# Kernel optimization log

Hardware: AMD Instinct MI355X
Metric: run time of the kernel (lower is better)

Reference implementation:

```python
import jax, jax.numpy as jnp
import numpy as np

H, T, D = 16, 2048, 1024
DH = D // H  # 64


def setup_inputs() -> dict:
    key = jax.random.key(0)
    ks = jax.random.split(key, 6)
    state = jax.random.normal(ks[0], (H, DH, DH), jnp.float32) * 0.02  # per-head recurrent state
    x = jax.random.normal(ks[1], (T, D), jnp.float32)
    done = jax.random.uniform(ks[2], (T,)) < (4.0 / T)  # sparse episode-reset flags (bool)
    w_qkv = jax.random.normal(ks[3], (D, 3 * D), jnp.float32) / np.sqrt(D)
    b_qkv = jnp.zeros((3 * D,), jnp.float32)
    w_out = jax.random.normal(ks[4], (D, D), jnp.float32) / np.sqrt(D)
    b_out = jnp.zeros((D,), jnp.float32)
    return {"state": state, "x": x, "done": done, "w_qkv": w_qkv,
            "b_qkv": b_qkv, "w_out": w_out, "b_out": b_out}


def _mha_forward(state, x, done, w_qkv, b_qkv, w_out, b_out):
    # qkv projection; einops 'T (QKV H Dh) -> QKV H T Dh'
    qkv = (x @ w_qkv + b_qkv).reshape(T, 3, H, DH).transpose(1, 2, 0, 3)
    q, k, v = qkv[0], qkv[1], qkv[2]  # each (H, T, Dh)

    cum = jnp.cumsum(done.astype(jnp.int32))  # inclusive cumsum, as in done.cumsum()
    before_first = cum == 0            # tokens before first reset (attend to carried state)
    after_last = cum == cum[-1]        # tokens after last reset (feed new state)
    done_any = cum[-1] > 0

    # make_attn_mask(done): causal AND no reset index i with s < i <= t.
    # The scanned mask equals: causal & (cum[t] == cum[s]) (same-segment).
    t_idx = jnp.arange(T)
    mask = (t_idx[:, None] >= t_idx[None, :]) & (cum[:, None] == cum[None, :])  # (T, T)

    attn = jnp.where(mask[None], jnp.einsum('htd,hsd->hts', q, k), 0.0)  # mask * (q @ k.T)
    q_bef = q * before_first[None, :, None]
    out = jnp.einsum('hts,hsd->htd', attn, v) + jnp.einsum('htd,hde->hte', q_bef, state)

    k_aft = k * after_last[None, :, None]
    v_aft = v * after_last[None, :, None]
    s_new = jnp.einsum('htd,hte->hde', k_aft, v_aft)  # k_aft.T @ v_aft per head
    new_state = jnp.where(done_any, s_new, state + s_new)

    # 'H T Dh -> T (H Dh)' then output projection
    x_out = out.transpose(1, 0, 2).reshape(T, D) @ w_out + b_out
    return new_state, x_out


def reference(state, x, done, w_qkv, b_qkv, w_out, b_out):
    return _mha_forward(state, x, done, w_qkv, b_qkv, w_out, b_out)
```

## Files before the change

kernel.cpp:

```cpp
#include <hip/hip_runtime.h>

#define TT 2048
#define DD 1024
#define HH 16
#define DH 64
#define QKV_N 3072
#define QKW 2048

typedef __attribute__((ext_vector_type(8))) short bf16x8;
typedef __attribute__((ext_vector_type(4))) short short4v;
typedef __attribute__((ext_vector_type(4))) float f32x4;

__device__ inline short f2bf(float f) {
    union { float f; unsigned u; } v; v.f = f;
    unsigned r = v.u + 0x7fff + ((v.u >> 16) & 1);
    return (short)(r >> 16);
}

__device__ inline f32x4 mfma16(bf16x8 a, bf16x8 b, f32x4 c) {
    return __builtin_amdgcn_mfma_f32_16x16x32_bf16(a, b, c, 0, 0, 0);
}

__device__ __forceinline__ void gload16(const void* g, void* l) {
    __builtin_amdgcn_global_load_lds(
        (const __attribute__((address_space(1))) unsigned int*)g,
        (__attribute__((address_space(3))) unsigned int*)l, 16, 0, 0);
}

__device__ void transpose_tile(const float* __restrict__ in, short* __restrict__ out,
                               int R, int C, int r0, int c0, float (*tile)[65]) {
    int tid = threadIdx.x;
#pragma unroll
    for (int p = 0; p < 4; ++p) {
        int ch = tid + p * 256;
        int r = ch >> 4, c4 = (ch & 15) * 4;
        float4 v = *(const float4*)&in[(size_t)(r0 + r) * C + c0 + c4];
        tile[r][c4] = v.x; tile[r][c4 + 1] = v.y; tile[r][c4 + 2] = v.z; tile[r][c4 + 3] = v.w;
    }
    __syncthreads();
#pragma unroll
    for (int p = 0; p < 2; ++p) {
        int ch = tid + p * 256;
        int c = ch >> 3, r8 = (ch & 7) * 8;
        short tmp[8];
#pragma unroll
        for (int i = 0; i < 8; ++i) tmp[i] = f2bf(tile[r8 + i][c]);
        *(float4*)&out[(size_t)(c0 + c) * R + r0 + r8] = *(float4*)tmp;
    }
}

__global__ __launch_bounds__(256) void prep_kernel(const float* __restrict__ x,
                                                   const float* __restrict__ w_qkv,
                                                   const float* __restrict__ w_out,
                                                   const float* __restrict__ state,
                                                   const int* __restrict__ done,
                                                   short* __restrict__ x_bf,
                                                   short* __restrict__ wqT,
                                                   short* __restrict__ woT,
                                                   short* __restrict__ stT,
                                                   float* __restrict__ stout,
                                                   int* __restrict__ seg,
                                                   int* __restrict__ totalp,
                                                   int* __restrict__ aux) {
    __shared__ float tile[64][65];
    __shared__ int scanbuf[2048 + 512 + 1];
    int b = blockIdx.x;
    int tid = threadIdx.x;
    if (b < 1024) {
        int i = (b * 256 + tid) * 8;
        float4 a = *(const float4*)&x[i];
        float4 c = *(const float4*)&x[i + 4];
        short tmp[8] = {f2bf(a.x), f2bf(a.y), f2bf(a.z), f2bf(a.w),
                        f2bf(c.x), f2bf(c.y), f2bf(c.z), f2bf(c.w)};
        *(float4*)&x_bf[i] = *(float4*)tmp;
    } else if (b < 1792) {
        int bb = b - 1024;
        transpose_tile(w_qkv, wqT, DD, QKV_N, (bb & 15) * 64, (bb >> 4) * 64, tile);
    } else if (b < 2048) {
        int bb = b - 1792;
        transpose_tile(w_out, woT, DD, DD, (bb & 15) * 64, (bb >> 4) * 64, tile);
    } else if (b < 2064) {
        int h = b - 2048;
        transpose_tile(state + (size_t)h * 4096, stT + (size_t)h * 4096, DH, DH, 0, 0, tile);
    } else if (b < 2128) {
        __shared__ int anyf;
        if (tid == 0) anyf = 0;
        __syncthreads();
        int acc = 0;
#pragma unroll
        for (int i = 0; i < 8; ++i) acc |= done[tid * 8 + i];
        if (acc) anyf = 1;
        __syncthreads();
        int f = ((b - 2064) * 256 + tid) * 4;
        float4 v = anyf ? make_float4(0.f, 0.f, 0.f, 0.f) : *(const float4*)&state[f];
        *(float4*)&stout[f] = v;
    } else {
        int* segl = scanbuf;
        int* part = scanbuf + 2048;
        int* excl = scanbuf + 2304;
        int base = tid * 8;
        int local[8];
        int run = 0;
#pragma unroll
        for (int i = 0; i < 8; ++i) { run += (done[base + i] != 0) ? 1 : 0; local[i] = run; }
        part[tid] = run;
        __syncthreads();
        if (tid < 64) {
            int p4[4];
#pragma unroll
            for (int i = 0; i < 4; ++i) p4[i] = part[tid * 4 + i];
            int s = p4[0] + p4[1] + p4[2] + p4[3];
            int v = s;
#pragma unroll
            for (int off = 1; off < 64; off <<= 1) {
                int u = __shfl_up(v, off);
                if (tid >= off) v += u;
            }
            int ex = v - s;
#pragma unroll
            for (int i = 0; i < 4; ++i) { excl[tid * 4 + i] = ex; ex += p4[i]; }
            if (tid == 63) { totalp[0] = v; scanbuf[2560] = v; }
        }
        __syncthreads();
        int off = excl[tid];
#pragma unroll
        for (int i = 0; i < 8; ++i) {
            int sv = off + local[i];
            seg[base + i] = sv;
            segl[base + i] = sv;
        }
        __syncthreads();
        if (tid < 33) {
            int target = (tid < 32) ? segl[tid * 64] : scanbuf[2560];
            int lo = 0, hi = 2047;
            while (lo < hi) { int mid = (lo + hi) >> 1; if (segl[mid] >= target) hi = mid; else lo = mid + 1; }
            aux[tid] = lo >> 6;
        }
    }
}

__global__ __launch_bounds__(256) void gemm_qkv(const short* __restrict__ A,
                                                const short* __restrict__ BT,
                                                const float* __restrict__ bias,
                                                short* __restrict__ qk,
                                                short* __restrict__ vt) {
    __shared__ __align__(16) short As[2][2][128 * 32];
    __shared__ __align__(16) short Bs[2][2][128 * 32];
    const int K = DD;
    int tid = threadIdx.x;
    int wave = tid >> 6, lane = tid & 63;
    int quad = lane >> 4, l15 = lane & 15;
    int m0 = blockIdx.x * 128, n0 = blockIdx.y * 128;
    int wr = (wave >> 1) * 64, wc = (wave & 1) * 64;

    int srow = wave * 32 + (lane >> 2);
    int scol = (lane & 3) * 8;
    const short* Ag = A + (size_t)(m0 + srow) * K + scol;
    const short* Bg = BT + (size_t)(n0 + srow) * K + scol;

#pragma unroll
    for (int g = 0; g < 2; ++g)
#pragma unroll
        for (int ks = 0; ks < 2; ++ks) {
            gload16(Ag + (size_t)g * 16 * K + ks * 32, &As[0][ks][(wave * 32 + g * 16) * 32]);
            gload16(Bg + (size_t)g * 16 * K + ks * 32, &Bs[0][ks][(wave * 32 + g * 16) * 32]);
        }
    __syncthreads();

    f32x4 acc[4][4] = {};
    int cur = 0;
    for (int k0 = 0; k0 < K; k0 += 64, cur ^= 1) {
        if (k0 + 64 < K) {
#pragma unroll
            for (int g = 0; g < 2; ++g)
#pragma unroll
                for (int ks = 0; ks < 2; ++ks) {
                    gload16(Ag + (size_t)g * 16 * K + k0 + 64 + ks * 32,
                            &As[cur ^ 1][ks][(wave * 32 + g * 16) * 32]);
                    gload16(Bg + (size_t)g * 16 * K + k0 + 64 + ks * 32,
                            &Bs[cur ^ 1][ks][(wave * 32 + g * 16) * 32]);
                }
        }
#pragma unroll
        for (int ks = 0; ks < 2; ++ks) {
            bf16x8 af[4], bfr[4];
#pragma unroll
            for (int i = 0; i < 4; ++i) {
                af[i]  = *(const bf16x8*)&As[cur][ks][(wr + i * 16 + l15) * 32 + quad * 8];
                bfr[i] = *(const bf16x8*)&Bs[cur][ks][(wc + i * 16 + l15) * 32 + quad * 8];
            }
#pragma unroll
            for (int i = 0; i < 4; ++i)
#pragma unroll
                for (int j = 0; j < 4; ++j)
                    acc[i][j] = mfma16(af[i], bfr[j], acc[i][j]);
        }
        __syncthreads();
    }

    if (n0 < 2048) {
#pragma unroll
        for (int i = 0; i < 4; ++i)
#pragma unroll
            for (int j = 0; j < 4; ++j)
#pragma unroll
                for (int r = 0; r < 4; ++r) {
                    int row = m0 + wr + i * 16 + quad * 4 + r;
                    int col = n0 + wc + j * 16 + l15;
                    qk[(size_t)row * QKW + col] = f2bf(acc[i][j][r] + bias[col]);
                }
    } else {
#pragma unroll
        for (int j = 0; j < 4; ++j) {
            int col = n0 + wc + j * 16 + l15;
            float bv = bias[col];
            int eg = col - 2048;
            int hh = eg >> 6, e = eg & 63;
#pragma unroll
            for (int i = 0; i < 4; ++i) {
                int tb = m0 + wr + i * 16 + quad * 4;
                short4v pk;
#pragma unroll
                for (int r = 0; r < 4; ++r) pk[r] = f2bf(acc[i][j][r] + bv);
                *(short4v*)&vt[(size_t)hh * (DH * TT) + (size_t)e * TT + tb] = pk;
            }
        }
    }
}

__global__ __launch_bounds__(256) void attn_mfma(const short* __restrict__ qk,
                                                 const short* __restrict__ vt,
                                                 const short* __restrict__ stT,
                                                 const int* __restrict__ seg,
                                                 const int* __restrict__ totalp,
                                                 const int* __restrict__ aux,
                                                 short* __restrict__ outb,
                                                 float* __restrict__ nsout) {
    __shared__ __align__(16) short Qh[2][64 * 32];
    __shared__ __align__(16) short Kh[2][2][64 * 32];
    __shared__ __align__(16) short Vh[2][2][64 * 32];
    __shared__ __align__(16) short Ss[64 * 72];

    int h = blockIdx.x, tt = blockIdx.y, z = blockIdx.z;
    int t0 = tt * 64;
    int tid = threadIdx.x, wave = tid >> 6, lane = tid & 63;
    int quad = lane >> 4, l15 = lane & 15;
    int myt = wave * 16;
    const short* vbase = vt + (size_t)h * (DH * TT);

    if (z == 1) {
        if (tt < aux[32]) return;
        int total = totalp[0];
        int myd = wave * 16;
        short* K0 = Kh[0][0];
        short* K1 = Kh[0][1];
        bool keep = (seg[t0 + lane] == total);
        const short* src = qk + (size_t)(t0 + lane) * QKW + 1024 + h * DH + myd;
        union { float4 f; short s[8]; } u0, u1;
        u0.f = keep ? *(const float4*)src : make_float4(0.f, 0.f, 0.f, 0.f);
        u1.f = keep ? *(const float4*)(src + 8) : make_float4(0.f, 0.f, 0.f, 0.f);
        short* dst = (lane < 32) ? &K0[lane] : &K1[lane - 32];
#pragma unroll
        for (int i = 0; i < 8; ++i) {
            dst[(myd + i) * 32] = u0.s[i];
            dst[(myd + 8 + i) * 32] = u1.s[i];
        }
        bf16x8 a0 = *(const bf16x8*)&K0[(myd + l15) * 32 + quad * 8];
        bf16x8 a1 = *(const bf16x8*)&K1[(myd + l15) * 32 + quad * 8];
        f32x4 acc2[4] = {};
#pragma unroll
        for (int j = 0; j < 4; ++j) {
            const short* vrow = vbase + (size_t)(j * 16 + l15) * TT + t0 + quad * 8;
            bf16x8 b0 = *(const bf16x8*)vrow;
            bf16x8 b1 = *(const bf16x8*)(vrow + 32);
            acc2[j] = mfma16(a0, b0, acc2[j]);
            acc2[j] = mfma16(a1, b1, acc2[j]);
        }
        float* oh = nsout + (size_t)h * 4096;
#pragma unroll
        for (int j = 0; j < 4; ++j)
#pragma unroll
            for (int r = 0; r < 4; ++r)
                atomicAdd(&oh[(myd + quad * 4 + r) * DH + j * 16 + l15], acc2[j][r]);
        return;
    }

    int st0 = aux[tt];
    int sr = lane >> 2;
    int ch = lane & 3;
    const short* kg = qk + 1024 + h * DH;

    {
#pragma unroll
        for (int h2 = 0; h2 < 2; ++h2)
            gload16(qk + (size_t)(t0 + myt + sr) * QKW + h * DH + h2 * 32 + ch * 8,
                    &Qh[h2][myt * 32]);
        int s0 = st0 * 64;
        gload16(kg + (size_t)(s0 + myt + sr) * QKW + ch * 8,      &Kh[0][0][myt * 32]);
        gload16(kg + (size_t)(s0 + myt + sr) * QKW + 32 + ch * 8, &Kh[0][1][myt * 32]);
        gload16(vbase + (size_t)(myt + sr) * TT + s0 + ch * 8,    &Vh[0][0][myt * 32]);
        gload16(vbase + (size_t)(myt + sr) * TT + s0 + 32 + ch * 8, &Vh[0][1][myt * 32]);
    }
    __syncthreads();

    bf16x8 af[2];
#pragma unroll
    for (int h2 = 0; h2 < 2; ++h2)
        af[h2] = *(const bf16x8*)&Qh[h2][(myt + l15) * 32 + quad * 8];

    int t_val = t0 + myt + l15;
    int seg_lane = seg[t_val];

    f32x4 acc2[4] = {};
    if (seg[t0] == 0) {
        const short* sb = stT + (size_t)h * 4096;
#pragma unroll
        for (int j = 0; j < 4; ++j)
#pragma unroll
            for (int h2 = 0; h2 < 2; ++h2) {
                bf16x8 a = *(const bf16x8*)(sb + (j * 16 + l15) * 64 + h2 * 32 + quad * 8);
                acc2[j] = mfma16(a, af[h2], acc2[j]);
            }
        if (seg_lane != 0) {
#pragma unroll
            for (int j = 0; j < 4; ++j)
#pragma unroll
                for (int r = 0; r < 4; ++r) acc2[j][r] = 0.f;
        }
    }

    int p = 0;
    for (int st = st0; st <= tt; ++st, p ^= 1) {
        if (st != st0) __syncthreads();
        if (st + 1 <= tt) {
            int s1 = (st + 1) * 64;
            gload16(kg + (size_t)(s1 + myt + sr) * QKW + ch * 8,        &Kh[p ^ 1][0][myt * 32]);
            gload16(kg + (size_t)(s1 + myt + sr) * QKW + 32 + ch * 8,   &Kh[p ^ 1][1][myt * 32]);
            gload16(vbase + (size_t)(myt + sr) * TT + s1 + ch * 8,      &Vh[p ^ 1][0][myt * 32]);
            gload16(vbase + (size_t)(myt + sr) * TT + s1 + 32 + ch * 8, &Vh[p ^ 1][1][myt * 32]);
        }
        int s0 = st * 64;

        f32x4 sacc[4] = {};
#pragma unroll
        for (int j = 0; j < 4; ++j)
#pragma unroll
            for (int h2 = 0; h2 < 2; ++h2) {
                bf16x8 kb = *(const bf16x8*)&Kh[p][h2][(j * 16 + l15) * 32 + quad * 8];
                sacc[j] = mfma16(kb, af[h2], sacc[j]);
            }
        int4 seg4[4];
#pragma unroll
        for (int j = 0; j < 4; ++j)
            seg4[j] = *(const int4*)&seg[s0 + j * 16 + quad * 4];
#pragma unroll
        for (int j = 0; j < 4; ++j) {
            short4v pk;
#pragma unroll
            for (int r = 0; r < 4; ++r) {
                int s_val = s0 + j * 16 + quad * 4 + r;
                int sv = (r == 0) ? seg4[j].x : (r == 1) ? seg4[j].y : (r == 2) ? seg4[j].z : seg4[j].w;
                bool ok = (sv == seg_lane) && (s_val <= t_val);
                pk[r] = ok ? f2bf(sacc[j][r]) : (short)0;
            }
            *(short4v*)&Ss[(myt + l15) * 72 + j * 16 + quad * 4] = pk;
        }
        bf16x8 sf[2];
#pragma unroll
        for (int h2 = 0; h2 < 2; ++h2)
            sf[h2] = *(const bf16x8*)&Ss[(myt + l15) * 72 + h2 * 32 + quad * 8];
#pragma unroll
        for (int j = 0; j < 4; ++j)
#pragma unroll
            for (int h2 = 0; h2 < 2; ++h2) {
                bf16x8 vb = *(const bf16x8*)&Vh[p][h2][(j * 16 + l15) * 32 + quad * 8];
                acc2[j] = mfma16(vb, sf[h2], acc2[j]);
            }
    }

#pragma unroll
    for (int j = 0; j < 4; ++j) {
        short4v pk;
#pragma unroll
        for (int r = 0; r < 4; ++r) pk[r] = f2bf(acc2[j][r]);
        *(short4v*)&outb[(size_t)t_val * DD + h * DH + j * 16 + quad * 4] = pk;
    }
}

__global__ __launch_bounds__(256) void gemm_out(const short* __restrict__ A,
                                                const short* __restrict__ BT,
                                                float* __restrict__ P,
                                                int M, int N, int K) {
    __shared__ __align__(16) short As[2][128 * 32];
    __shared__ __align__(16) short Bs[2][128 * 32];
    int tid = threadIdx.x;
    int wave = tid >> 6, lane = tid & 63;
    int quad = lane >> 4, l15 = lane & 15;
    int m0 = blockIdx.x * 128, n0 = blockIdx.y * 128;
    int kb0 = blockIdx.z * (K / 2), kb1 = kb0 + K / 2;
    int wr = (wave >> 1) * 64, wc = (wave & 1) * 64;

    int srow = wave * 16 + (lane >> 2);
    int scol = (lane & 3) * 8;
    const short* Ag = A + (size_t)(m0 + srow) * K + scol;
    const short* Bg = BT + (size_t)(n0 + srow) * K + scol;
    float* Pz = P + (size_t)blockIdx.z * TT * DD;

    gload16(Ag + kb0, &As[0][(wave * 16) * 32]);
    gload16(Ag + (size_t)64 * K + kb0, &As[0][(64 + wave * 16) * 32]);
    gload16(Bg + kb0, &Bs[0][(wave * 16) * 32]);
    gload16(Bg + (size_t)64 * K + kb0, &Bs[0][(64 + wave * 16) * 32]);
    __syncthreads();

    f32x4 acc[4][4] = {};
    int cur = 0;
    for (int k0 = kb0; k0 < kb1; k0 += 32, cur ^= 1) {
        if (k0 + 32 < kb1) {
            gload16(Ag + k0 + 32, &As[cur ^ 1][(wave * 16) * 32]);
            gload16(Ag + (size_t)64 * K + k0 + 32, &As[cur ^ 1][(64 + wave * 16) * 32]);
            gload16(Bg + k0 + 32, &Bs[cur ^ 1][(wave * 16) * 32]);
            gload16(Bg + (size_t)64 * K + k0 + 32, &Bs[cur ^ 1][(64 + wave * 16) * 32]);
        }
        bf16x8 af[4], bfr[4];
#pragma unroll
        for (int i = 0; i < 4; ++i) {
            af[i]  = *(const bf16x8*)&As[cur][(wr + i * 16 + l15) * 32 + quad * 8];
            bfr[i] = *(const bf16x8*)&Bs[cur][(wc + i * 16 + l15) * 32 + quad * 8];
        }
#pragma unroll
        for (int i = 0; i < 4; ++i)
#pragma unroll
            for (int j = 0; j < 4; ++j)
                acc[i][j] = mfma16(af[i], bfr[j], acc[i][j]);
        __syncthreads();
    }
#pragma unroll
    for (int i = 0; i < 4; ++i)
#pragma unroll
        for (int j = 0; j < 4; ++j)
#pragma unroll
            for (int r = 0; r < 4; ++r) {
                int row = m0 + wr + i * 16 + quad * 4 + r;
                int col = n0 + wc + j * 16 + l15;
                Pz[(size_t)row * N + col] = acc[i][j][r];
            }
}

__global__ __launch_bounds__(256) void reduce_out(const float* __restrict__ P,
                                                  const float* __restrict__ bias,
                                                  float* __restrict__ x_out) {
    int f = (blockIdx.x * 256 + threadIdx.x) * 4;
    int col = f & (DD - 1);
    float4 a = *(const float4*)&P[f];
    float4 b = *(const float4*)&P[(size_t)TT * DD + f];
    float4 c = *(const float4*)&bias[col];
    float4 o = make_float4(a.x + b.x + c.x, a.y + b.y + c.y,
                           a.z + b.z + c.z, a.w + b.w + c.w);
    *(float4*)&x_out[f] = o;
}

extern "C" void kernel_launch(void* const* d_in, const int* in_sizes, int n_in,
                              void* d_out, int out_size, void* d_ws, size_t ws_size,
                              hipStream_t stream) {
    const float* state = (const float*)d_in[0];
    const float* x     = (const float*)d_in[1];
    const int*   done  = (const int*)d_in[2];
    const float* w_qkv = (const float*)d_in[3];
    const float* b_qkv = (const float*)d_in[4];
    const float* w_out = (const float*)d_in[5];
    const float* b_out = (const float*)d_in[6];

    char* ws = (char*)d_ws;
    int*   seg    = (int*)ws;
    int*   totalp = (int*)(ws + 8192);
    int*   aux    = (int*)(ws + 8256);
    short* wqT    = (short*)(ws + 8448);
    short* woT    = (short*)(ws + 6299904);
    short* stT    = (short*)(ws + 8397056);
    short* qk     = (short*)(ws + 8528128);
    short* vt     = (short*)(ws + 16916736);
    short* xbf_outb = (short*)(ws + 21111040);
    float* Pout   = (float*)(ws + 25305344);

    float* new_state_out = (float*)d_out;
    float* x_out         = (float*)d_out + HH * DH * DH;

    prep_kernel<<<2129, 256, 0, stream>>>(x, w_qkv, w_out, state, done,
                                          xbf_outb, wqT, woT, stT,
                                          new_state_out, seg, totalp, aux);

    gemm_qkv<<<dim3(TT / 128, QKV_N / 128), 256, 0, stream>>>(
        xbf_outb, wqT, b_qkv, qk, vt);

    attn_mfma<<<dim3(HH, TT / 64, 2), 256, 0, stream>>>(
        qk, vt, stT, seg, totalp, aux, xbf_outb, new_state_out);

    gemm_out<<<dim3(TT / 128, DD / 128, 2), 256, 0, stream>>>(
        xbf_outb, woT, Pout, TT, DD, DD);

    reduce_out<<<2048, 256, 0, stream>>>(Pout, b_out, x_out);
}
```

Measured before the change: 152.8 us.

## Shrink GEMM M-tiles to 64 and drop split-K reduction for output projection

The QKV GEMM moves from 128x128 to 64x128 tiles, doubling the block count to 768, and gains a launch-bounds occupancy hint. The output-projection GEMM drops its split-K=2 scheme and the separate reduce kernel in favour of 64x128 tiles over the full K with BK=64, adding the bias directly in the epilogue. This removes the fp32 partial-sum round trip through memory and one kernel launch, and balances the grid better across CUs. The cost is less operand reuse per block and more per-block K iterations for the output GEMM.

```diff
diff --git a/kernel.cpp b/kernel.cpp
--- a/kernel.cpp
+++ b/kernel.cpp
@@ -139,58 +139,56 @@
     }
 }
 
-__global__ __launch_bounds__(256) void gemm_qkv(const short* __restrict__ A,
-                                                const short* __restrict__ BT,
-                                                const float* __restrict__ bias,
-                                                short* __restrict__ qk,
-                                                short* __restrict__ vt) {
-    __shared__ __align__(16) short As[2][2][128 * 32];
+__global__ __launch_bounds__(256, 3) void gemm_qkv(const short* __restrict__ A,
+                                                   const short* __restrict__ BT,
+                                                   const float* __restrict__ bias,
+                                                   short* __restrict__ qk,
+                                                   short* __restrict__ vt) {
+    __shared__ __align__(16) short As[2][2][64 * 32];
     __shared__ __align__(16) short Bs[2][2][128 * 32];
     const int K = DD;
     int tid = threadIdx.x;
     int wave = tid >> 6, lane = tid & 63;
     int quad = lane >> 4, l15 = lane & 15;
-    int m0 = blockIdx.x * 128, n0 = blockIdx.y * 128;
-    int wr = (wave >> 1) * 64, wc = (wave & 1) * 64;
-
-    int srow = wave * 32 + (lane >> 2);
+    int m0 = blockIdx.x * 64, n0 = blockIdx.y * 128;
+    int wr = (wave >> 1) * 32, wc = (wave & 1) * 64;
+
+    int srow = wave * 16 + (lane >> 2);
     int scol = (lane & 3) * 8;
     const short* Ag = A + (size_t)(m0 + srow) * K + scol;
     const short* Bg = BT + (size_t)(n0 + srow) * K + scol;
 
 #pragma unroll
-    for (int g = 0; g < 2; ++g)
-#pragma unroll
-        for (int ks = 0; ks < 2; ++ks) {
-            gload16(Ag + (size_t)g * 16 * K + ks * 32, &As[0][ks][(wave * 32 + g * 16) * 32]);
-            gload16(Bg + (size_t)g * 16 * K + ks * 32, &Bs[0][ks][(wave * 32 + g * 16) * 32]);
-        }
+    for (int ks = 0; ks < 2; ++ks) {
+        gload16(Ag + ks * 32, &As[0][ks][(wave * 16) * 32]);
+        gload16(Bg + ks * 32, &Bs[0][ks][(wave * 16) * 32]);
+        gload16(Bg + (size_t)64 * K + ks * 32, &Bs[0][ks][(64 + wave * 16) * 32]);
+    }
     __syncthreads();
 
-    f32x4 acc[4][4] = {};
+    f32x4 acc[2][4] = {};
     int cur = 0;
     for (int k0 = 0; k0 < K; k0 += 64, cur ^= 1) {
         if (k0 + 64 < K) {
 #pragma unroll
-            for (int g = 0; g < 2; ++g)
-#pragma unroll
-                for (int ks = 0; ks < 2; ++ks) {
-                    gload16(Ag + (size_t)g * 16 * K + k0 + 64 + ks * 32,
-                            &As[cur ^ 1][ks][(wave * 32 + g * 16) * 32]);
-                    gload16(Bg + (size_t)g * 16 * K + k0 + 64 + ks * 32,
-                            &Bs[cur ^ 1][ks][(wave * 32 + g * 16) * 32]);
-                }
+            for (int ks = 0; ks < 2; ++ks) {
+                gload16(Ag + k0 + 64 + ks * 32, &As[cur ^ 1][ks][(wave * 16) * 32]);
+                gload16(Bg + k0 + 64 + ks * 32, &Bs[cur ^ 1][ks][(wave * 16) * 32]);
+                gload16(Bg + (size_t)64 * K + k0 + 64 + ks * 32,
+                        &Bs[cur ^ 1][ks][(64 + wave * 16) * 32]);
+            }
         }
 #pragma unroll
         for (int ks = 0; ks < 2; ++ks) {
-            bf16x8 af[4], bfr[4];
-#pragma unroll
-            for (int i = 0; i < 4; ++i) {
+            bf16x8 af[2], bfr[4];
+#pragma unroll
+            for (int i = 0; i < 2; ++i)
                 af[i]  = *(const bf16x8*)&As[cur][ks][(wr + i * 16 + l15) * 32 + quad * 8];
-                bfr[i] = *(const bf16x8*)&Bs[cur][ks][(wc + i * 16 + l15) * 32 + quad * 8];
-            }
-#pragma unroll
-            for (int i = 0; i < 4; ++i)
+#pragma unroll
+            for (int j = 0; j < 4; ++j)
+                bfr[j] = *(const bf16x8*)&Bs[cur][ks][(wc + j * 16 + l15) * 32 + quad * 8];
+#pragma unroll
+            for (int i = 0; i < 2; ++i)
 #pragma unroll
                 for (int j = 0; j < 4; ++j)
                     acc[i][j] = mfma16(af[i], bfr[j], acc[i][j]);
@@ -200,7 +198,7 @@
 
     if (n0 < 2048) {
 #pragma unroll
-        for (int i = 0; i < 4; ++i)
+        for (int i = 0; i < 2; ++i)
 #pragma unroll
             for (int j = 0; j < 4; ++j)
 #pragma unroll
@@ -217,7 +215,7 @@
             int eg = col - 2048;
             int hh = eg >> 6, e = eg & 63;
 #pragma unroll
-            for (int i = 0; i < 4; ++i) {
+            for (int i = 0; i < 2; ++i) {
                 int tb = m0 + wr + i * 16 + quad * 4;
                 short4v pk;
 #pragma unroll
@@ -389,74 +387,72 @@
 
 __global__ __launch_bounds__(256) void gemm_out(const short* __restrict__ A,
                                                 const short* __restrict__ BT,
-                                                float* __restrict__ P,
-                                                int M, int N, int K) {
-    __shared__ __align__(16) short As[2][128 * 32];
-    __shared__ __align__(16) short Bs[2][128 * 32];
+                                                const float* __restrict__ bias,
+                                                float* __restrict__ x_out) {
+    __shared__ __align__(16) short As[2][2][64 * 32];
+    __shared__ __align__(16) short Bs[2][2][128 * 32];
+    const int K = DD, N = DD;
     int tid = threadIdx.x;
     int wave = tid >> 6, lane = tid & 63;
     int quad = lane >> 4, l15 = lane & 15;
-    int m0 = blockIdx.x * 128, n0 = blockIdx.y * 128;
-    int kb0 = blockIdx.z * (K / 2), kb1 = kb0 + K / 2;
-    int wr = (wave >> 1) * 64, wc = (wave & 1) * 64;
+    int m0 = blockIdx.x * 64, n0 = blockIdx.y * 128;
+    int wr = (wave >> 1) * 32, wc = (wave & 1) * 64;
 
     int srow = wave * 16 + (lane >> 2);
     int scol = (lane & 3) * 8;
     const short* Ag = A + (size_t)(m0 + srow) * K + scol;
     const short* Bg = BT + (size_t)(n0 + srow) * K + scol;
-    float* Pz = P + (size_t)blockIdx.z * TT * DD;
-
-    gload16(Ag + kb0, &As[0][(wave * 16) * 32]);
-    gload16(Ag + (size_t)64 * K + kb0, &As[0][(64 + wave * 16) * 32]);
-    gload16(Bg + kb0, &Bs[0][(wave * 16) * 32]);
-    gload16(Bg + (size_t)64 * K + kb0, &Bs[0][(64 + wave * 16) * 32]);
+
+#pragma unroll
+    for (int ks = 0; ks < 2; ++ks) {
+        gload16(Ag + ks * 32, &As[0][ks][(wave * 16) * 32]);
+        gload16(Bg + ks * 32, &Bs[0][ks][(wave * 16) * 32]);
+        gload16(Bg + (size_t)64 * K + ks * 32, &Bs[0][ks][(64 + wave * 16) * 32]);
+    }
     __syncthreads();
 
-    f32x4 acc[4][4] = {};
+    f32x4 acc[2][4] = {};
     int cur = 0;
-    for (int k0 = kb0; k0 < kb1; k0 += 32, cur ^= 1) {
-        if (k0 + 32 < kb1) {
-            gload16(Ag + k0 + 32, &As[cur ^ 1][(wave * 16) * 32]);
-            gload16(Ag + (size_t)64 * K + k0 + 32, &As[cur ^ 1][(64 + wave * 16) * 32]);
-            gload16(Bg + k0 + 32, &Bs[cur ^ 1][(wave * 16) * 32]);
-            gload16(Bg + (size_t)64 * K + k0 + 32, &Bs[cur ^ 1][(64 + wave * 16) * 32]);
-        }
-        bf16x8 af[4], bfr[4];
-#pragma unroll
-        for (int i = 0; i < 4; ++i) {
-            af[i]  = *(const bf16x8*)&As[cur][(wr + i * 16 + l15) * 32 + quad * 8];
-            bfr[i] = *(const bf16x8*)&Bs[cur][(wc + i * 16 + l15) * 32 + quad * 8];
-        }
-#pragma unroll
-        for (int i = 0; i < 4; ++i)
+    for (int k0 = 0; k0 < K; k0 += 64, cur ^= 1) {
+        if (k0 + 64 < K) {
+#pragma unroll
+            for (int ks = 0; ks < 2; ++ks) {
+                gload16(Ag + k0 + 64 + ks * 32, &As[cur ^ 1][ks][(wave * 16) * 32]);
+                gload16(Bg + k0 + 64 + ks * 32, &Bs[cur ^ 1][ks][(wave * 16) * 32]);
+                gload16(Bg + (size_t)64 * K + k0 + 64 + ks * 32,
+                        &Bs[cur ^ 1][ks][(64 + wave * 16) * 32]);
+            }
+        }
+#pragma unroll
+        for (int ks = 0; ks < 2; ++ks) {
+            bf16x8 af[2], bfr[4];
+#pragma unroll
+            for (int i = 0; i < 2; ++i)
+                af[i]  = *(const bf16x8*)&As[cur][ks][(wr + i * 16 + l15) * 32 + quad * 8];
 #pragma unroll
             for (int j = 0; j < 4; ++j)
-                acc[i][j] = mfma16(af[i], bfr[j], acc[i][j]);
-        __syncthreads();
-    }
-#pragma unroll
-    for (int i = 0; i < 4; ++i)
-#pragma unroll
-        for (int j = 0; j < 4; ++j)
+                bfr[j] = *(const bf16x8*)&Bs[cur][ks][(wc + j * 16 + l15) * 32 + quad * 8];
+#pragma unroll
+            for (int i = 0; i < 2; ++i)
+#pragma unroll
+                for (int j = 0; j < 4; ++j)
+                    acc[i][j] = mfma16(af[i], bfr[j], acc[i][j]);
+        }
+        __syncthreads();
+    }
+
+#pragma unroll
+    for (int i = 0; i < 2; ++i)
+#pragma unroll
+        for (int j = 0; j < 4; ++j) {
+            int col = n0 + wc + j * 16 + l15;
+            float bv = bias[col];
 #pragma unroll
             for (int r = 0; r < 4; ++r) {
                 int row = m0 + wr + i * 16 + quad * 4 + r;
-                int col = n0 + wc + j * 16 + l15;
-                Pz[(size_t)row * N + col] = acc[i][j][r];
-            }
-}
-
-__global__ __launch_bounds__(256) void reduce_out(const float* __restrict__ P,
-                                                  const float* __restrict__ bias,
-                                                  float* __restrict__ x_out) {
-    int f = (blockIdx.x * 256 + threadIdx.x) * 4;
-    int col = f & (DD - 1);
-    float4 a = *(const float4*)&P[f];
-    float4 b = *(const float4*)&P[(size_t)TT * DD + f];
-    float4 c = *(const float4*)&bias[col];
-    float4 o = make_float4(a.x + b.x + c.x, a.y + b.y + c.y,
-                           a.z + b.z + c.z, a.w + b.w + c.w);
-    *(float4*)&x_out[f] = o;
+                x_out[(size_t)row * N + col] = acc[i][j][r] + bv;
+            }
+        }
 }
 
 extern "C" void kernel_launch(void* const* d_in, const int* in_sizes, int n_in,
@@ -480,7 +476,6 @@
     short* qk     = (short*)(ws + 8528128);
     short* vt     = (short*)(ws + 16916736);
     short* xbf_outb = (short*)(ws + 21111040);
-    float* Pout   = (float*)(ws + 25305344);
 
     float* new_state_out = (float*)d_out;
     float* x_out         = (float*)d_out + HH * DH * DH;
@@ -489,14 +484,12 @@
                                           xbf_outb, wqT, woT, stT,
                                           new_state_out, seg, totalp, aux);
 
-    gemm_qkv<<<dim3(TT / 128, QKV_N / 128), 256, 0, stream>>>(
+    gemm_qkv<<<dim3(TT / 64, QKV_N / 128), 256, 0, stream>>>(
         xbf_outb, wqT, b_qkv, qk, vt);
 
     attn_mfma<<<dim3(HH, TT / 64, 2), 256, 0, stream>>>(
         qk, vt, stT, seg, totalp, aux, xbf_outb, new_state_out);
 
-    gemm_out<<<dim3(TT / 128, DD / 128, 2), 256, 0, stream>>>(
-        xbf_outb, woT, Pout, TT, DD, DD);
-
-    reduce_out<<<2048, 256, 0, stream>>>(Pout, b_out, x_out);
-}
+    gemm_out<<<dim3(TT / 64, DD / 128), 256, 0, stream>>>(
+        xbf_outb, woT, b_out, x_out);
+}
```

New measurement: 147.2 us, median of 2. 1.04x faster.
